# Optimization experiments

Hardware: AMD Instinct MI355X
Metric: run time of the kernel (lower is better)

Reference implementation:

```python
import jax, jax.numpy as jnp
import numpy as np

N_EMB = 512
N_HEADS = 8
HEAD_SIZE = N_EMB // N_HEADS  # 64
B, T = 4, 2048
EPS = 1e-5


def layernorm(x, g, b):
    mu = jnp.mean(x, axis=-1, keepdims=True)
    var = jnp.var(x, axis=-1, keepdims=True)
    return (x - mu) * jax.lax.rsqrt(var + EPS) * g + b


def setup_inputs() -> dict:
    key = jax.random.key(0)
    ks = jax.random.split(key, 8)
    s = 1.0 / np.sqrt(N_EMB)
    x = jax.random.normal(ks[0], (B, T, N_EMB), dtype=jnp.float32)
    # per-head q/k/v weights stacked: [H, n_emb, head_size]
    wq = jax.random.uniform(ks[1], (N_HEADS, N_EMB, HEAD_SIZE), minval=-s, maxval=s, dtype=jnp.float32)
    wk = jax.random.uniform(ks[2], (N_HEADS, N_EMB, HEAD_SIZE), minval=-s, maxval=s, dtype=jnp.float32)
    wv = jax.random.uniform(ks[3], (N_HEADS, N_EMB, HEAD_SIZE), minval=-s, maxval=s, dtype=jnp.float32)
    w_ff = jax.random.uniform(ks[4], (N_EMB, N_EMB), minval=-s, maxval=s, dtype=jnp.float32)
    b_ff = jax.random.uniform(ks[5], (N_EMB,), minval=-s, maxval=s, dtype=jnp.float32)
    ln1_g = jnp.ones((N_EMB,), jnp.float32)
    ln1_b = jnp.zeros((N_EMB,), jnp.float32)
    ln2_g = jnp.ones((N_EMB,), jnp.float32)
    ln2_b = jnp.zeros((N_EMB,), jnp.float32)
    return {"x": x, "wq": wq, "wk": wk, "wv": wv, "w_ff": w_ff, "b_ff": b_ff,
            "ln1_g": ln1_g, "ln1_b": ln1_b, "ln2_g": ln2_g, "ln2_b": ln2_b}


def reference(x, wq, wk, wv, w_ff, b_ff, ln1_g, ln1_b, ln2_g, ln2_b):
    # --- self-attention branch (dropout=0 -> identity) ---
    h = layernorm(x, ln1_g, ln1_b)                       # [B,T,C]
    q = jnp.einsum('btc,hcd->bhtd', h, wq)               # [B,H,T,d]
    k = jnp.einsum('btc,hcd->bhtd', h, wk)
    v = jnp.einsum('btc,hcd->bhtd', h, wv)
    scale = HEAD_SIZE ** -0.5
    wei = jnp.einsum('bhtd,bhsd->bhts', q, k) * scale    # [B,H,T,T]
    Tt = x.shape[1]
    causal = jnp.tril(jnp.ones((Tt, Tt), dtype=bool))
    wei = jnp.where(causal, wei, -jnp.inf)
    wei = jax.nn.softmax(wei, axis=-1)
    attn = jnp.einsum('bhts,bhsd->bhtd', wei, v)         # [B,H,T,d]
    # concat heads along last dim (head order preserved)
    Bn, H, Tn, d = attn.shape
    sa = jnp.transpose(attn, (0, 2, 1, 3)).reshape(Bn, Tn, H * d)
    x = x + sa
    # --- feed-forward branch: Linear + ReLU (dropout=0) ---
    h2 = layernorm(x, ln2_g, ln2_b)
    ff = jax.nn.relu(h2 @ w_ff + b_ff)
    return x + ff
```

## Files before the change

### kernel.cpp

```cpp
#include <hip/hip_runtime.h>

#define Bsz  4
#define Tseq 2048
#define Cdim 512
#define Hn   8
#define Dh   64
#define BT   8192
#define NQKV 1536
#define NEG_BIG (-1e30f)

typedef __attribute__((ext_vector_type(8))) short bf16x8;
typedef __attribute__((ext_vector_type(4))) short bf16x4;
typedef __attribute__((ext_vector_type(4))) float f32x4;

__device__ __forceinline__ float b2f(short s) {
    unsigned u = ((unsigned)(unsigned short)s) << 16;
    float f; __builtin_memcpy(&f, &u, 4); return f;
}
__device__ __forceinline__ short f2b(float f) {
    unsigned u; __builtin_memcpy(&u, &f, 4);
    u = (u + 0x7fffu + ((u >> 16) & 1u)) >> 16;
    return (short)u;
}
__device__ __forceinline__ void g2l16(const short* g, short* l) {
    __builtin_amdgcn_global_load_lds(
        (const __attribute__((address_space(1))) unsigned int*)(uintptr_t)g,
        (__attribute__((address_space(3))) unsigned int*)l, 16, 0, 0);
}

__global__ __launch_bounds__(256) void k_prep(const float* __restrict__ wq, const float* __restrict__ wk,
                                              const float* __restrict__ wv, const float* __restrict__ wff,
                                              short* __restrict__ wqkvt, short* __restrict__ wfft,
                                              const float* __restrict__ x, const float* __restrict__ g,
                                              const float* __restrict__ b, short* __restrict__ out) {
    const int blk = blockIdx.x, tid = threadIdx.x;
    if (blk < 256) {
        __shared__ float ldsT[64 * 65];
        if (blk < 192) {
            int hm = blk >> 3, ct = blk & 7;
            int proj = hm >> 3, h = hm & 7;
            const float* w = (proj == 0) ? wq : (proj == 1 ? wk : wv);
#pragma unroll
            for (int i = 0; i < 16; i++) {
                int flat = i * 256 + tid, cc = flat >> 6, dd = flat & 63;
                ldsT[dd * 65 + cc] = w[(h * 512 + ct * 64 + cc) * 64 + dd];
            }
            __syncthreads();
#pragma unroll
            for (int i = 0; i < 16; i++) {
                int flat = i * 256 + tid, dd = flat >> 6, cc = flat & 63;
                int n = proj * 512 + h * 64 + dd;
                wqkvt[n * 512 + ct * 64 + cc] = f2b(ldsT[dd * 65 + cc]);
            }
        } else {
            int b2 = blk - 192, rt = b2 >> 3, nt8 = b2 & 7;
#pragma unroll
            for (int i = 0; i < 16; i++) {
                int flat = i * 256 + tid, cc = flat >> 6, nn = flat & 63;
                ldsT[nn * 65 + cc] = wff[(rt * 64 + cc) * 512 + nt8 * 64 + nn];
            }
            __syncthreads();
#pragma unroll
            for (int i = 0; i < 16; i++) {
                int flat = i * 256 + tid, nn = flat >> 6, cc = flat & 63;
                wfft[(nt8 * 64 + nn) * 512 + rt * 64 + cc] = f2b(ldsT[nn * 65 + cc]);
            }
        }
    } else {
        int row  = (blk - 256) * 4 + (tid >> 6);
        int lane = tid & 63;
        const f32x4 a0 = *(const f32x4*)(x + row * Cdim + lane * 8);
        const f32x4 a1 = *(const f32x4*)(x + row * Cdim + lane * 8 + 4);
        float v[8] = {a0[0], a0[1], a0[2], a0[3], a1[0], a1[1], a1[2], a1[3]};
        float s = 0.f, sq = 0.f;
#pragma unroll
        for (int i = 0; i < 8; i++) { s += v[i]; sq += v[i] * v[i]; }
#pragma unroll
        for (int off = 1; off < 64; off <<= 1) { s += __shfl_xor(s, off); sq += __shfl_xor(sq, off); }
        float mean = s * (1.f / 512.f);
        float var  = sq * (1.f / 512.f) - mean * mean;
        float rstd = rsqrtf(var + 1e-5f);
        const f32x4 g0 = *(const f32x4*)(g + lane * 8);
        const f32x4 g1 = *(const f32x4*)(g + lane * 8 + 4);
        const f32x4 b0 = *(const f32x4*)(b + lane * 8);
        const f32x4 b1 = *(const f32x4*)(b + lane * 8 + 4);
        float gg[8] = {g0[0], g0[1], g0[2], g0[3], g1[0], g1[1], g1[2], g1[3]};
        float bb[8] = {b0[0], b0[1], b0[2], b0[3], b1[0], b1[1], b1[2], b1[3]};
        bf16x8 o;
#pragma unroll
        for (int i = 0; i < 8; i++) o[i] = f2b((v[i] - mean) * rstd * gg[i] + bb[i]);
        *(bf16x8*)(out + row * Cdim + lane * 8) = o;
    }
}

__global__ __launch_bounds__(256) void k_ln(const float* __restrict__ x, const float* __restrict__ g,
                                            const float* __restrict__ b, short* __restrict__ out) {
    int row  = blockIdx.x * 4 + (threadIdx.x >> 6);
    int lane = threadIdx.x & 63;
    const f32x4 a0 = *(const f32x4*)(x + row * Cdim + lane * 8);
    const f32x4 a1 = *(const f32x4*)(x + row * Cdim + lane * 8 + 4);
    float v[8] = {a0[0], a0[1], a0[2], a0[3], a1[0], a1[1], a1[2], a1[3]};
    float s = 0.f, sq = 0.f;
#pragma unroll
    for (int i = 0; i < 8; i++) { s += v[i]; sq += v[i] * v[i]; }
#pragma unroll
    for (int off = 1; off < 64; off <<= 1) { s += __shfl_xor(s, off); sq += __shfl_xor(sq, off); }
    float mean = s * (1.f / 512.f);
    float var  = sq * (1.f / 512.f) - mean * mean;
    float rstd = rsqrtf(var + 1e-5f);
    const f32x4 g0 = *(const f32x4*)(g + lane * 8);
    const f32x4 g1 = *(const f32x4*)(g + lane * 8 + 4);
    const f32x4 b0 = *(const f32x4*)(b + lane * 8);
    const f32x4 b1 = *(const f32x4*)(b + lane * 8 + 4);
    float gg[8] = {g0[0], g0[1], g0[2], g0[3], g1[0], g1[1], g1[2], g1[3]};
    float bb[8] = {b0[0], b0[1], b0[2], b0[3], b1[0], b1[1], b1[2], b1[3]};
    bf16x8 o;
#pragma unroll
    for (int i = 0; i < 8; i++) o[i] = f2b((v[i] - mean) * rstd * gg[i] + bb[i]);
    *(bf16x8*)(out + row * Cdim + lane * 8) = o;
}

__global__ __launch_bounds__(256) void k_gemm_qkv(const short* __restrict__ A, const short* __restrict__ Wt,
                                                  short* __restrict__ q, short* __restrict__ k,
                                                  short* __restrict__ vt) {
    const int tid = threadIdx.x;
    const int wave = tid >> 6, lane = tid & 63;
    const int quad = lane >> 4, l15 = lane & 15;
    const int m0 = blockIdx.x * 128, n0 = blockIdx.y * 128;
    const int wm = wave & 1, wn = wave >> 1;
    __shared__ __align__(16) short As[128 * 32];
    __shared__ __align__(16) short Bs[128 * 32];
    f32x4 acc[4][4];
#pragma unroll
    for (int i = 0; i < 4; i++)
#pragma unroll
        for (int j = 0; j < 4; j++) acc[i][j] = (f32x4){0.f, 0.f, 0.f, 0.f};
    const int lr = lane >> 2, lc = lane & 3;
    const short* Ag = A  + (m0 + wave * 32 + lr) * Cdim + lc * 8;
    const short* Bg = Wt + (n0 + wave * 32 + lr) * Cdim + lc * 8;
    short* Al = As + wave * 1024;
    short* Bl = Bs + wave * 1024;
    for (int kk = 0; kk < 16; kk++) {
        const int k0 = kk * 32;
        g2l16(Ag + k0,             Al);
        g2l16(Ag + 16 * Cdim + k0, Al + 512);
        g2l16(Bg + k0,             Bl);
        g2l16(Bg + 16 * Cdim + k0, Bl + 512);
        __syncthreads();
        bf16x8 a[4], w[4];
#pragma unroll
        for (int mt = 0; mt < 4; mt++) a[mt] = *(const bf16x8*)(As + (wm * 64 + mt * 16 + l15) * 32 + quad * 8);
#pragma unroll
        for (int nt = 0; nt < 4; nt++) w[nt] = *(const bf16x8*)(Bs + (wn * 64 + nt * 16 + l15) * 32 + quad * 8);
#pragma unroll
        for (int mt = 0; mt < 4; mt++)
#pragma unroll
            for (int nt = 0; nt < 4; nt++)
                acc[mt][nt] = __builtin_amdgcn_mfma_f32_16x16x32_bf16(a[mt], w[nt], acc[mt][nt], 0, 0, 0);
        __syncthreads();
    }
    const int proj = n0 >> 9;
    const int n0w  = n0 + wn * 64;
    const int hh   = (n0w & 511) >> 6;
    const int m0w  = m0 + wm * 64;
#pragma unroll
    for (int mt = 0; mt < 4; mt++) {
#pragma unroll
        for (int r = 0; r < 4; r++) {
            int t  = m0w + mt * 16 + quad * 4 + r;
            int bi = t >> 11, tt = t & 2047;
#pragma unroll
            for (int nt = 0; nt < 4; nt++) {
                int d = nt * 16 + l15;
                short val = f2b(acc[mt][nt][r]);
                if (proj == 0)      q [((bi * Hn + hh) * Tseq + tt) * Dh + d] = val;
                else if (proj == 1) k [((bi * Hn + hh) * Tseq + tt) * Dh + d] = val;
                else                vt[((bi * Hn + hh) * Dh + d) * Tseq + tt] = val;
            }
        }
    }
}

__global__ __launch_bounds__(256, 3) void k_attn(const short* __restrict__ qb, const short* __restrict__ kb,
                                                 const short* __restrict__ vtb, const float* __restrict__ x,
                                                 float* __restrict__ out1) {
    const int wave = threadIdx.x >> 6, lane = threadIdx.x & 63;
    const int quad = lane >> 4, l15 = lane & 15;
    const int D  = blockIdx.y * 32 + blockIdx.x;
    const int j5 = D & 31;
    const int bh = (j5 & 7) * 4 + (j5 >> 3);
    const int u  = D >> 5, kq = u >> 3, d8 = u & 7;
    const int qg = (kq == 0) ? 31 - d8 : (kq == 1) ? 16 + d8 : (kq == 2) ? 15 - d8 : d8;
    const int q0  = qg * 64;
    const int qw0 = q0 + wave * 16;
    const int nkt = qg + 1;

    const short* Q = qb  + bh * Tseq * Dh;
    const short* K = kb  + bh * Tseq * Dh;
    const short* V = vtb + bh * Dh * Tseq;

    __shared__ __align__(16) short Ks[2][64 * 64];
    __shared__ __align__(16) short Vs[2][64 * 64];
    __shared__ __align__(16) short Ps[4][16 * 72];
    short* pw = &Ps[wave][0];

    const int lr8 = lane >> 3, lc8 = lane & 7;
    const int sw8 = (lc8 ^ lr8) << 3;
    const short* Ksrc = K + (wave * 16 + lr8) * Dh + sw8;
    const short* Vsrc = V + (wave * 16 + lr8) * Tseq + sw8;

    g2l16(Ksrc,            &Ks[0][wave * 1024]);
    g2l16(Ksrc + 8 * Dh,   &Ks[0][wave * 1024 + 512]);
    g2l16(Vsrc,            &Vs[0][wave * 1024]);
    g2l16(Vsrc + 8 * Tseq, &Vs[0][wave * 1024 + 512]);

    bf16x8 qa[2];
#pragma unroll
    for (int c = 0; c < 2; c++)
        qa[c] = *(const bf16x8*)(Q + (qw0 + l15) * Dh + c * 32 + quad * 8);

    f32x4 o[4];
#pragma unroll
    for (int i = 0; i < 4; i++) o[i] = (f32x4){0.f, 0.f, 0.f, 0.f};
    float m_i = NEG_BIG, l_i = 0.f;

    const float sc = 0.125f * 1.44269504089f;
    const int sx = l15 & 7;

    __syncthreads();

    for (int kt = 0; kt < nkt; kt++) {
        const short* Kb = &Ks[kt & 1][0];
        const short* Vb = &Vs[kt & 1][0];
        if (kt + 1 < nkt) {
            g2l16(Ksrc + (kt + 1) * 64 * Dh,            &Ks[(kt + 1) & 1][wave * 1024]);
            g2l16(Ksrc + (kt + 1) * 64 * Dh + 8 * Dh,   &Ks[(kt + 1) & 1][wave * 1024 + 512]);
            g2l16(Vsrc + (kt + 1) * 64,                 &Vs[(kt + 1) & 1][wave * 1024]);
            g2l16(Vsrc + (kt + 1) * 64 + 8 * Tseq,      &Vs[(kt + 1) & 1][wave * 1024 + 512]);
        }
        const int s0 = kt * 64;
        f32x4 st[4];
#pragma unroll
        for (int nt = 0; nt < 4; nt++) {
            bf16x8 k0 = *(const bf16x8*)(Kb + (nt * 16 + l15) * 64 + ((quad ^ sx) << 3));
            bf16x8 k1 = *(const bf16x8*)(Kb + (nt * 16 + l15) * 64 + (((4 | quad) ^ sx) << 3));
            f32x4 z = (f32x4){0.f, 0.f, 0.f, 0.f};
            z = __builtin_amdgcn_mfma_f32_16x16x32_bf16(k0, qa[0], z, 0, 0, 0);
            z = __builtin_amdgcn_mfma_f32_16x16x32_bf16(k1, qa[1], z, 0, 0, 0);
            st[nt] = z;
        }
        const int qq = qw0 + l15;
        if (kt == nkt - 1) {
#pragma unroll
            for (int nt = 0; nt < 4; nt++)
#pragma unroll
                for (int r = 0; r < 4; r++) {
                    int s = s0 + nt * 16 + quad * 4 + r;
                    st[nt][r] = (s > qq) ? NEG_BIG : st[nt][r] * sc;
                }
        } else {
#pragma unroll
            for (int nt = 0; nt < 4; nt++)
#pragma unroll
                for (int r = 0; r < 4; r++) st[nt][r] *= sc;
        }
        float mx = fmaxf(fmaxf(fmaxf(st[0][0], st[0][1]), fmaxf(st[0][2], st[0][3])),
                         fmaxf(fmaxf(st[1][0], st[1][1]), fmaxf(st[1][2], st[1][3])));
        mx = fmaxf(mx, fmaxf(fmaxf(fmaxf(st[2][0], st[2][1]), fmaxf(st[2][2], st[2][3])),
                             fmaxf(fmaxf(st[3][0], st[3][1]), fmaxf(st[3][2], st[3][3]))));
        mx = fmaxf(mx, __shfl_xor(mx, 16));
        mx = fmaxf(mx, __shfl_xor(mx, 32));
        float mn    = fmaxf(m_i, mx);
        float alpha = __builtin_amdgcn_exp2f(m_i - mn);
        m_i = mn;
        float rs = 0.f;
        bf16x4 pk[4];
#pragma unroll
        for (int nt = 0; nt < 4; nt++) {
#pragma unroll
            for (int r = 0; r < 4; r++) {
                float p = __builtin_amdgcn_exp2f(st[nt][r] - mn);
                rs += p;
                pk[nt][r] = f2b(p);
            }
        }
        rs += __shfl_xor(rs, 16);
        rs += __shfl_xor(rs, 32);
        l_i = l_i * alpha + rs;
#pragma unroll
        for (int nt = 0; nt < 4; nt++)
            *(bf16x4*)(pw + l15 * 72 + nt * 16 + quad * 4) = pk[nt];
#pragma unroll
        for (int r = 0; r < 4; r++) {
            float ar = __shfl(alpha, quad * 4 + r);
#pragma unroll
            for (int dt = 0; dt < 4; dt++) o[dt][r] *= ar;
        }
        asm volatile("s_waitcnt lgkmcnt(0)" ::: "memory");
        bf16x8 pa[2];
#pragma unroll
        for (int c = 0; c < 2; c++)
            pa[c] = *(const bf16x8*)(pw + l15 * 72 + c * 32 + quad * 8);
#pragma unroll
        for (int c = 0; c < 2; c++)
#pragma unroll
            for (int v4 = 0; v4 < 4; v4++) {
                bf16x8 vb = *(const bf16x8*)(Vb + (v4 * 16 + l15) * 64 + ((((c << 2) | quad) ^ sx) << 3));
                o[v4] = __builtin_amdgcn_mfma_f32_16x16x32_bf16(pa[c], vb, o[v4], 0, 0, 0);
            }
        __syncthreads();
    }
    const int bi = bh >> 3, hh = bh & 7;
#pragma unroll
    for (int r = 0; r < 4; r++) {
        int row = quad * 4 + r;
        float Lr  = __shfl(l_i, row);
        float inv = 1.f / Lr;
#pragma unroll
        for (int v4 = 0; v4 < 4; v4++) {
            int t   = qw0 + row;
            int idx = (bi * Tseq + t) * Cdim + hh * Dh + v4 * 16 + l15;
            out1[idx] = x[idx] + o[v4][r] * inv;
        }
    }
}

__global__ __launch_bounds__(256) void k_gemm_ff(const short* __restrict__ A, const short* __restrict__ Wt,
                                                 const float* __restrict__ bias, const float* __restrict__ res,
                                                 float* __restrict__ out) {
    const int tid = threadIdx.x;
    const int wave = tid >> 6, lane = tid & 63;
    const int quad = lane >> 4, l15 = lane & 15;
    const int m0 = blockIdx.x * 128, n0 = blockIdx.y * 128;
    const int wm = wave & 1, wn = wave >> 1;
    __shared__ __align__(16) short As[128 * 32];
    __shared__ __align__(16) short Bs[128 * 32];
    f32x4 acc[4][4];
#pragma unroll
    for (int i = 0; i < 4; i++)
#pragma unroll
        for (int j = 0; j < 4; j++) acc[i][j] = (f32x4){0.f, 0.f, 0.f, 0.f};
    const int lr = lane >> 2, lc = lane & 3;
    const short* Ag = A  + (m0 + wave * 32 + lr) * Cdim + lc * 8;
    const short* Bg = Wt + (n0 + wave * 32 + lr) * Cdim + lc * 8;
    short* Al = As + wave * 1024;
    short* Bl = Bs + wave * 1024;
    for (int kk = 0; kk < 16; kk++) {
        const int k0 = kk * 32;
        g2l16(Ag + k0,             Al);
        g2l16(Ag + 16 * Cdim + k0, Al + 512);
        g2l16(Bg + k0,             Bl);
        g2l16(Bg + 16 * Cdim + k0, Bl + 512);
        __syncthreads();
        bf16x8 a[4], w[4];
#pragma unroll
        for (int mt = 0; mt < 4; mt++) a[mt] = *(const bf16x8*)(As + (wm * 64 + mt * 16 + l15) * 32 + quad * 8);
#pragma unroll
        for (int nt = 0; nt < 4; nt++) w[nt] = *(const bf16x8*)(Bs + (wn * 64 + nt * 16 + l15) * 32 + quad * 8);
#pragma unroll
        for (int mt = 0; mt < 4; mt++)
#pragma unroll
            for (int nt = 0; nt < 4; nt++)
                acc[mt][nt] = __builtin_amdgcn_mfma_f32_16x16x32_bf16(a[mt], w[nt], acc[mt][nt], 0, 0, 0);
        __syncthreads();
    }
    const int m0w = m0 + wm * 64, n0w = n0 + wn * 64;
#pragma unroll
    for (int mt = 0; mt < 4; mt++) {
#pragma unroll
        for (int r = 0; r < 4; r++) {
            int t = m0w + mt * 16 + quad * 4 + r;
#pragma unroll
            for (int nt = 0; nt < 4; nt++) {
                int n = n0w + nt * 16 + l15;
                float fv = acc[mt][nt][r] + bias[n];
                fv = fmaxf(fv, 0.f);
                out[t * Cdim + n] = res[t * Cdim + n] + fv;
            }
        }
    }
}

extern "C" void kernel_launch(void* const* d_in, const int* in_sizes, int n_in,
                              void* d_out, int out_size, void* d_ws, size_t ws_size,
                              hipStream_t stream) {
    const float* x   = (const float*)d_in[0];
    const float* wq  = (const float*)d_in[1];
    const float* wk  = (const float*)d_in[2];
    const float* wv  = (const float*)d_in[3];
    const float* wff = (const float*)d_in[4];
    const float* bff = (const float*)d_in[5];
    const float* g1  = (const float*)d_in[6];
    const float* b1  = (const float*)d_in[7];
    const float* g2  = (const float*)d_in[8];
    const float* b2  = (const float*)d_in[9];

    char* p = (char*)d_ws;
    short* wqkvt = (short*)p; p += (size_t)NQKV * Cdim * 2;
    short* wfft  = (short*)p; p += (size_t)Cdim * Cdim * 2;
    short* h1    = (short*)p; p += (size_t)BT * Cdim * 2;
    short* qb    = (short*)p; p += (size_t)BT * Cdim * 2;
    short* kb    = (short*)p; p += (size_t)BT * Cdim * 2;
    short* vtb   = (short*)p; p += (size_t)BT * Cdim * 2;
    float* out1  = (float*)p; p += (size_t)BT * Cdim * 4;

    hipLaunchKernelGGL(k_prep,     dim3(2304),    dim3(256), 0, stream,
                       wq, wk, wv, wff, wqkvt, wfft, x, g1, b1, h1);
    hipLaunchKernelGGL(k_gemm_qkv, dim3(64, 12),  dim3(256), 0, stream, h1, wqkvt, qb, kb, vtb);
    hipLaunchKernelGGL(k_attn,     dim3(32, 32),  dim3(256), 0, stream, qb, kb, vtb, x, out1);
    hipLaunchKernelGGL(k_ln,       dim3(2048),    dim3(256), 0, stream, out1, g2, b2, h1);
    hipLaunchKernelGGL(k_gemm_ff,  dim3(64, 4),   dim3(256), 0, stream, h1, wfft, bff, out1, (float*)d_out);
}
```

Measured before the change: 180.7 us.

## Double-buffer LDS tiles in QKV and FF GEMMs; halve FF N-tile

Both GEMM kernels now use two LDS buffers and prefetch the next K-slice while computing the current one, which removes one barrier per iteration and overlaps global loads with MFMA work. The FF GEMM's N tile shrinks from 128 to 64, doubling the grid to 512 blocks so the machine's compute units are better filled. Costs are double the LDS footprint, which may lower occupancy, and more A-tile reloads in the FF GEMM. Whether g2l16 is synchronous affects how much overlap actually happens.

```diff
diff --git a/kernel.cpp b/kernel.cpp
--- a/kernel.cpp
+++ b/kernel.cpp
@@ -128,8 +128,8 @@
     const int quad = lane >> 4, l15 = lane & 15;
     const int m0 = blockIdx.x * 128, n0 = blockIdx.y * 128;
     const int wm = wave & 1, wn = wave >> 1;
-    __shared__ __align__(16) short As[128 * 32];
-    __shared__ __align__(16) short Bs[128 * 32];
+    __shared__ __align__(16) short As[2][128 * 32];
+    __shared__ __align__(16) short Bs[2][128 * 32];
     f32x4 acc[4][4];
 #pragma unroll
     for (int i = 0; i < 4; i++)
@@ -138,20 +138,25 @@
     const int lr = lane >> 2, lc = lane & 3;
     const short* Ag = A  + (m0 + wave * 32 + lr) * Cdim + lc * 8;
     const short* Bg = Wt + (n0 + wave * 32 + lr) * Cdim + lc * 8;
-    short* Al = As + wave * 1024;
-    short* Bl = Bs + wave * 1024;
+    g2l16(Ag,             &As[0][wave * 1024]);
+    g2l16(Ag + 16 * Cdim, &As[0][wave * 1024 + 512]);
+    g2l16(Bg,             &Bs[0][wave * 1024]);
+    g2l16(Bg + 16 * Cdim, &Bs[0][wave * 1024 + 512]);
+    __syncthreads();
     for (int kk = 0; kk < 16; kk++) {
-        const int k0 = kk * 32;
-        g2l16(Ag + k0,             Al);
-        g2l16(Ag + 16 * Cdim + k0, Al + 512);
-        g2l16(Bg + k0,             Bl);
-        g2l16(Bg + 16 * Cdim + k0, Bl + 512);
-        __syncthreads();
+        const int cur = kk & 1, nxt = cur ^ 1;
+        if (kk + 1 < 16) {
+            const int k0 = (kk + 1) * 32;
+            g2l16(Ag + k0,             &As[nxt][wave * 1024]);
+            g2l16(Ag + 16 * Cdim + k0, &As[nxt][wave * 1024 + 512]);
+            g2l16(Bg + k0,             &Bs[nxt][wave * 1024]);
+            g2l16(Bg + 16 * Cdim + k0, &Bs[nxt][wave * 1024 + 512]);
+        }
         bf16x8 a[4], w[4];
 #pragma unroll
-        for (int mt = 0; mt < 4; mt++) a[mt] = *(const bf16x8*)(As + (wm * 64 + mt * 16 + l15) * 32 + quad * 8);
-#pragma unroll
-        for (int nt = 0; nt < 4; nt++) w[nt] = *(const bf16x8*)(Bs + (wn * 64 + nt * 16 + l15) * 32 + quad * 8);
+        for (int mt = 0; mt < 4; mt++) a[mt] = *(const bf16x8*)(&As[cur][(wm * 64 + mt * 16 + l15) * 32 + quad * 8]);
+#pragma unroll
+        for (int nt = 0; nt < 4; nt++) w[nt] = *(const bf16x8*)(&Bs[cur][(wn * 64 + nt * 16 + l15) * 32 + quad * 8]);
 #pragma unroll
         for (int mt = 0; mt < 4; mt++)
 #pragma unroll
@@ -331,47 +336,50 @@
     const int tid = threadIdx.x;
     const int wave = tid >> 6, lane = tid & 63;
     const int quad = lane >> 4, l15 = lane & 15;
-    const int m0 = blockIdx.x * 128, n0 = blockIdx.y * 128;
+    const int m0 = blockIdx.x * 128, n0 = blockIdx.y * 64;
     const int wm = wave & 1, wn = wave >> 1;
-    __shared__ __align__(16) short As[128 * 32];
-    __shared__ __align__(16) short Bs[128 * 32];
-    f32x4 acc[4][4];
+    __shared__ __align__(16) short As[2][128 * 32];
+    __shared__ __align__(16) short Bs[2][64 * 32];
+    f32x4 acc[4][2];
 #pragma unroll
     for (int i = 0; i < 4; i++)
 #pragma unroll
-        for (int j = 0; j < 4; j++) acc[i][j] = (f32x4){0.f, 0.f, 0.f, 0.f};
+        for (int j = 0; j < 2; j++) acc[i][j] = (f32x4){0.f, 0.f, 0.f, 0.f};
     const int lr = lane >> 2, lc = lane & 3;
     const short* Ag = A  + (m0 + wave * 32 + lr) * Cdim + lc * 8;
-    const short* Bg = Wt + (n0 + wave * 32 + lr) * Cdim + lc * 8;
-    short* Al = As + wave * 1024;
-    short* Bl = Bs + wave * 1024;
+    const short* Bg = Wt + (n0 + wave * 16 + lr) * Cdim + lc * 8;
+    g2l16(Ag,             &As[0][wave * 1024]);
+    g2l16(Ag + 16 * Cdim, &As[0][wave * 1024 + 512]);
+    g2l16(Bg,             &Bs[0][wave * 512]);
+    __syncthreads();
     for (int kk = 0; kk < 16; kk++) {
-        const int k0 = kk * 32;
-        g2l16(Ag + k0,             Al);
-        g2l16(Ag + 16 * Cdim + k0, Al + 512);
-        g2l16(Bg + k0,             Bl);
-        g2l16(Bg + 16 * Cdim + k0, Bl + 512);
-        __syncthreads();
-        bf16x8 a[4], w[4];
-#pragma unroll
-        for (int mt = 0; mt < 4; mt++) a[mt] = *(const bf16x8*)(As + (wm * 64 + mt * 16 + l15) * 32 + quad * 8);
-#pragma unroll
-        for (int nt = 0; nt < 4; nt++) w[nt] = *(const bf16x8*)(Bs + (wn * 64 + nt * 16 + l15) * 32 + quad * 8);
+        const int cur = kk & 1, nxt = cur ^ 1;
+        if (kk + 1 < 16) {
+            const int k0 = (kk + 1) * 32;
+            g2l16(Ag + k0,             &As[nxt][wave * 1024]);
+            g2l16(Ag + 16 * Cdim + k0, &As[nxt][wave * 1024 + 512]);
+            g2l16(Bg + k0,             &Bs[nxt][wave * 512]);
+        }
+        bf16x8 a[4], w[2];
+#pragma unroll
+        for (int mt = 0; mt < 4; mt++) a[mt] = *(const bf16x8*)(&As[cur][(wm * 64 + mt * 16 + l15) * 32 + quad * 8]);
+#pragma unroll
+        for (int nt = 0; nt < 2; nt++) w[nt] = *(const bf16x8*)(&Bs[cur][(wn * 32 + nt * 16 + l15) * 32 + quad * 8]);
 #pragma unroll
         for (int mt = 0; mt < 4; mt++)
 #pragma unroll
-            for (int nt = 0; nt < 4; nt++)
+            for (int nt = 0; nt < 2; nt++)
                 acc[mt][nt] = __builtin_amdgcn_mfma_f32_16x16x32_bf16(a[mt], w[nt], acc[mt][nt], 0, 0, 0);
         __syncthreads();
     }
-    const int m0w = m0 + wm * 64, n0w = n0 + wn * 64;
+    const int m0w = m0 + wm * 64, n0w = n0 + wn * 32;
 #pragma unroll
     for (int mt = 0; mt < 4; mt++) {
 #pragma unroll
         for (int r = 0; r < 4; r++) {
             int t = m0w + mt * 16 + quad * 4 + r;
 #pragma unroll
-            for (int nt = 0; nt < 4; nt++) {
+            for (int nt = 0; nt < 2; nt++) {
                 int n = n0w + nt * 16 + l15;
                 float fv = acc[mt][nt][r] + bias[n];
                 fv = fmaxf(fv, 0.f);
@@ -409,5 +417,5 @@
     hipLaunchKernelGGL(k_gemm_qkv, dim3(64, 12),  dim3(256), 0, stream, h1, wqkvt, qb, kb, vtb);
     hipLaunchKernelGGL(k_attn,     dim3(32, 32),  dim3(256), 0, stream, qb, kb, vtb, x, out1);
     hipLaunchKernelGGL(k_ln,       dim3(2048),    dim3(256), 0, stream, out1, g2, b2, h1);
-    hipLaunchKernelGGL(k_gemm_ff,  dim3(64, 4),   dim3(256), 0, stream, h1, wfft, bff, out1, (float*)d_out);
-}
+    hipLaunchKernelGGL(k_gemm_ff,  dim3(64, 8),   dim3(256), 0, stream, h1, wfft, bff, out1, (float*)d_out);
+}
```

Measured after the change: 172.9 us. 1.05x faster.
